# Performance work log

Measured on AMD Instinct MI355X. Metric: run time of the kernel, lower is better.

Reference implementation:

```python
import jax, jax.numpy as jnp
import numpy as np

H = 16   # n_heads == n_I
D = 64   # d_q = d_k = d_v = d_r
DX = H * D
B, S = 4, 2048

def setup_inputs() -> dict:
    key = jax.random.key(0)
    ks = jax.random.split(key, 9)
    sc = 0.02
    return {
        "value": jax.random.normal(ks[0], (B, S, DX), jnp.float32),
        "key":   jax.random.normal(ks[1], (B, S, DX), jnp.float32),
        "query": jax.random.normal(ks[2], (B, S, DX), jnp.float32),
        "Wq_w": jax.random.normal(ks[3], (DX, DX), jnp.float32) * sc,
        "Wq_b": jnp.zeros((DX,), jnp.float32),
        "Wk_w": jax.random.normal(ks[4], (DX, DX), jnp.float32) * sc,
        "Wk_b": jnp.zeros((DX,), jnp.float32),
        "Wv_w": jax.random.normal(ks[5], (DX, DX), jnp.float32) * sc,
        "Wv_b": jnp.zeros((DX,), jnp.float32),
        "Wr_w": jax.random.normal(ks[6], (DX, DX), jnp.float32) * sc,
        "Wr_b": jnp.zeros((DX,), jnp.float32),
        "Wout_w": jax.random.normal(ks[7], (DX, DX), jnp.float32) * sc,
        "Wout_b": jnp.zeros((DX,), jnp.float32),
    }

def _heads(x, b, s):
    # [b, s, H*D] -> [b, H, s, D]
    return x.reshape(b, s, H, D).transpose(0, 2, 1, 3)

def reference(value, key, query, Wq_w, Wq_b, Wk_w, Wk_b, Wv_w, Wv_b,
              Wr_w, Wr_b, Wout_w, Wout_b):
    b, s, _ = query.shape
    # torch nn.Linear: y = x @ W.T + b
    Q = _heads(query @ Wq_w.T + Wq_b, b, s)   # [b,H,s,D]
    K = _heads(key   @ Wk_w.T + Wk_b, b, s)
    V = _heads(value @ Wv_w.T + Wv_b, b, s)
    R = _heads(query @ Wr_w.T + Wr_b, b, s)
    dot_scale = jnp.sqrt(jnp.float32(D))
    scores = jnp.einsum("bhid,bhjd->bhij", Q, K) / dot_scale  # [b,H,s,s]
    attn = jax.nn.softmax(scores, axis=-1)                    # dropout p=0
    out = jnp.einsum("bhij,bhjd->bhid", attn, V)              # [b,H,s,D]
    out = out * R                                             # R-gating
    out = out.transpose(0, 2, 1, 3).reshape(b, s, H * D)
    return out @ Wout_w.T + Wout_b
```

## Files before the change

### kernel.cpp

```cpp
#include <hip/hip_runtime.h>
#include <hip/hip_bf16.h>

typedef __bf16 bf16;
typedef __bf16 bf16x4 __attribute__((ext_vector_type(4)));
typedef __bf16 bf16x8 __attribute__((ext_vector_type(8)));
typedef float  f32x4  __attribute__((ext_vector_type(4)));

#define MFMA_16x16x32(a, b, c) __builtin_amdgcn_mfma_f32_16x16x32_bf16((a), (b), (c), 0, 0, 0)

typedef const void __attribute__((address_space(1))) gvoid;
typedef void __attribute__((address_space(3))) svoid;

__device__ __forceinline__ void async_copy16(const void* gptr, void* ldsptr) {
    __builtin_amdgcn_global_load_lds((gvoid*)gptr, (svoid*)ldsptr, 16, 0, 0);
}

__global__ void cvt_f32_bf16(const float* __restrict__ src, bf16* __restrict__ dst, int n4)
{
    int i = blockIdx.x * blockDim.x + threadIdx.x;
    const int stride = gridDim.x * blockDim.x;
    for (; i < n4; i += stride) {
        float4 v = ((const float4*)src)[i];
        bf16x4 o = { (bf16)v.x, (bf16)v.y, (bf16)v.z, (bf16)v.w };
        ((bf16x4*)dst)[i] = o;
    }
}

template <typename OutT, bool TRANS>
__global__ void gemm_nt_bias(const bf16* __restrict__ X, const bf16* __restrict__ W,
                             const float* __restrict__ bias, OutT* __restrict__ Y,
                             int M, int N, int K)
{
    constexpr int SDIM = 2048;
    __shared__ alignas(16) bf16 As[128 * 32];
    __shared__ alignas(16) bf16 Bs[128 * 32];

    const int tid  = threadIdx.x;
    const int lane = tid & 63;
    const int wave = tid >> 6;
    const int wm   = wave >> 1;
    const int wn   = wave & 1;
    const int bm   = blockIdx.x * 128;
    const int bn   = blockIdx.y * 128;
    const int l15  = lane & 15;
    const int quad = lane >> 4;

    const int srow = lane >> 2;
    const int scol = (lane & 3) * 8;

    const bf16* aseg0 = X + (size_t)(bm + wave * 32 + srow) * K + scol;
    const bf16* aseg1 = X + (size_t)(bm + wave * 32 + 16 + srow) * K + scol;
    const bf16* bseg0 = W + (size_t)(bn + wave * 32 + srow) * K + scol;
    const bf16* bseg1 = W + (size_t)(bn + wave * 32 + 16 + srow) * K + scol;
    bf16* as0 = As + (wave * 2 + 0) * 512;
    bf16* as1 = As + (wave * 2 + 1) * 512;
    bf16* bs0 = Bs + (wave * 2 + 0) * 512;
    bf16* bs1 = Bs + (wave * 2 + 1) * 512;

    f32x4 acc[4][4] = {};

    for (int k0 = 0; k0 < K; k0 += 32) {
        __syncthreads();
        async_copy16(aseg0 + k0, as0);
        async_copy16(aseg1 + k0, as1);
        async_copy16(bseg0 + k0, bs0);
        async_copy16(bseg1 + k0, bs1);
        __syncthreads();

        bf16x8 af[4], bfr[4];
        #pragma unroll
        for (int i = 0; i < 4; ++i)
            af[i] = *(const bf16x8*)(As + (wm * 64 + i * 16 + l15) * 32 + quad * 8);
        #pragma unroll
        for (int j = 0; j < 4; ++j)
            bfr[j] = *(const bf16x8*)(Bs + (wn * 64 + j * 16 + l15) * 32 + quad * 8);
        #pragma unroll
        for (int i = 0; i < 4; ++i)
            #pragma unroll
            for (int j = 0; j < 4; ++j)
                acc[i][j] = MFMA_16x16x32(af[i], bfr[j], acc[i][j]);
    }

    #pragma unroll
    for (int i = 0; i < 4; ++i) {
        const int rowg = bm + wm * 64 + i * 16 + quad * 4;
        #pragma unroll
        for (int j = 0; j < 4; ++j) {
            const int colg = bn + wn * 64 + j * 16 + l15;
            const float bv = bias[colg];
            if (TRANS) {
                bf16x4 o;
                #pragma unroll
                for (int r = 0; r < 4; ++r) o[r] = (bf16)(acc[i][j][r] + bv);
                *(bf16x4*)((bf16*)Y + (size_t)(rowg >> 11) * N * SDIM
                                    + (size_t)colg * SDIM + (rowg & (SDIM - 1))) = o;
            } else {
                #pragma unroll
                for (int r = 0; r < 4; ++r)
                    Y[(size_t)(rowg + r) * N + colg] = (OutT)(acc[i][j][r] + bv);
            }
        }
    }
}

__launch_bounds__(256, 2)
__global__ void attn_fused(const bf16* __restrict__ Qp, const bf16* __restrict__ Kp,
                           const bf16* __restrict__ Vtp, const bf16* __restrict__ Rp,
                           bf16* __restrict__ Op)
{
    constexpr int S = 2048, DXc = 1024, Dh = 64;
    constexpr int PST = 88;
    __shared__ alignas(16) bf16 KsLo[64 * 32], KsHi[64 * 32];
    __shared__ alignas(16) bf16 VtLo[64 * 32], VtHi[64 * 32];
    __shared__ alignas(16) bf16 Pw[4][16 * PST];

    const int tid  = threadIdx.x;
    const int lane = tid & 63;
    const int wave = tid >> 6;
    const int qt = blockIdx.x, h = blockIdx.y, b = blockIdx.z;
    const int l15  = lane & 15;
    const int quad = lane >> 4;

    const size_t headbase = ((size_t)b * S) * DXc + h * Dh;
    const size_t vtbase   = ((size_t)(b * 16 + h) * Dh) * S;

    bf16x8 qf[4][2];
    #pragma unroll
    for (int mi = 0; mi < 4; ++mi) {
        const int qrow = qt * 256 + wave * 64 + mi * 16 + l15;
        const bf16* qptr = Qp + headbase + (size_t)qrow * DXc + quad * 8;
        qf[mi][0] = *(const bf16x8*)(qptr);
        qf[mi][1] = *(const bf16x8*)(qptr + 32);
        #pragma unroll
        for (int j = 0; j < 8; ++j) {
            qf[mi][0][j] = (bf16)((float)qf[mi][0][j] * 0.125f);
            qf[mi][1][j] = (bf16)((float)qf[mi][1][j] * 0.125f);
        }
    }

    f32x4 oacc[4][4] = {};
    float lsum[4][4] = {};

    const int srow = lane >> 2;
    const int scol = (lane & 3) * 8;
    const bf16* kseg = Kp  + headbase + (size_t)(16 * wave + srow) * DXc + scol;
    const bf16* vseg = Vtp + vtbase   + (size_t)(16 * wave + srow) * S   + scol;
    bf16* ksl = KsLo + wave * 512;
    bf16* ksh = KsHi + wave * 512;
    bf16* vtl = VtLo + wave * 512;
    bf16* vth = VtHi + wave * 512;
    bf16* pw  = &Pw[wave][0];

    for (int kv0 = 0; kv0 < S; kv0 += 64) {
        __syncthreads();
        async_copy16(kseg + (size_t)kv0 * DXc,      ksl);
        async_copy16(kseg + (size_t)kv0 * DXc + 32, ksh);
        async_copy16(vseg + kv0,                    vtl);
        async_copy16(vseg + kv0 + 32,               vth);
        __syncthreads();

        bf16x8 kf[4][2], vf[4][2];
        #pragma unroll
        for (int nb = 0; nb < 4; ++nb) {
            kf[nb][0] = *(const bf16x8*)(KsLo + (nb * 16 + l15) * 32 + quad * 8);
            kf[nb][1] = *(const bf16x8*)(KsHi + (nb * 16 + l15) * 32 + quad * 8);
            vf[nb][0] = *(const bf16x8*)(VtLo + (nb * 16 + l15) * 32 + quad * 8);
            vf[nb][1] = *(const bf16x8*)(VtHi + (nb * 16 + l15) * 32 + quad * 8);
        }

        #pragma unroll
        for (int mi = 0; mi < 4; ++mi) {
            f32x4 sacc[4];
            #pragma unroll
            for (int nb = 0; nb < 4; ++nb) {
                f32x4 z = {0.f, 0.f, 0.f, 0.f};
                z = MFMA_16x16x32(qf[mi][1], kf[nb][1], z);
                sacc[nb] = MFMA_16x16x32(qf[mi][0], kf[nb][0], z);
            }
            #pragma unroll
            for (int nb = 0; nb < 4; ++nb) {
                #pragma unroll
                for (int r = 0; r < 4; ++r) {
                    float p = __expf(sacc[nb][r]);
                    bf16 pb = (bf16)p;
                    lsum[mi][r] += (float)pb;
                    pw[(quad * 4 + r) * PST + nb * 16 + l15] = pb;
                }
            }
            bf16x8 pf0 = *(const bf16x8*)(pw + l15 * PST + quad * 8);
            bf16x8 pf1 = *(const bf16x8*)(pw + l15 * PST + 32 + quad * 8);
            #pragma unroll
            for (int db = 0; db < 4; ++db) {
                oacc[mi][db] = MFMA_16x16x32(pf0, vf[db][0], oacc[mi][db]);
                oacc[mi][db] = MFMA_16x16x32(pf1, vf[db][1], oacc[mi][db]);
            }
        }
    }

    #pragma unroll
    for (int m = 1; m < 16; m <<= 1)
        #pragma unroll
        for (int mi = 0; mi < 4; ++mi)
            #pragma unroll
            for (int r = 0; r < 4; ++r)
                lsum[mi][r] += __shfl_xor(lsum[mi][r], m, 64);

    #pragma unroll
    for (int mi = 0; mi < 4; ++mi) {
        #pragma unroll
        for (int r = 0; r < 4; ++r) {
            const float inv = 1.0f / lsum[mi][r];
            const int srowg = qt * 256 + wave * 64 + mi * 16 + quad * 4 + r;
            const size_t base = headbase + (size_t)srowg * DXc;
            #pragma unroll
            for (int db = 0; db < 4; ++db) {
                const int d = db * 16 + l15;
                const float o = oacc[mi][db][r] * inv;
                const float rg = (float)Rp[base + d];
                Op[base + d] = (bf16)(o * rg);
            }
        }
    }
}

extern "C" void kernel_launch(void* const* d_in, const int* in_sizes, int n_in,
                              void* d_out, int out_size, void* d_ws, size_t ws_size,
                              hipStream_t stream)
{
    (void)in_sizes; (void)n_in; (void)out_size; (void)ws_size;
    constexpr int B = 4, S = 2048, DX = 1024, M = B * S;
    constexpr size_t MD = (size_t)M * DX;
    constexpr size_t WD = (size_t)DX * DX;

    const float* value  = (const float*)d_in[0];
    const float* keyi   = (const float*)d_in[1];
    const float* query  = (const float*)d_in[2];
    const float* Wq_w   = (const float*)d_in[3];
    const float* Wq_b   = (const float*)d_in[4];
    const float* Wk_w   = (const float*)d_in[5];
    const float* Wk_b   = (const float*)d_in[6];
    const float* Wv_w   = (const float*)d_in[7];
    const float* Wv_b   = (const float*)d_in[8];
    const float* Wr_w   = (const float*)d_in[9];
    const float* Wr_b   = (const float*)d_in[10];
    const float* Wout_w = (const float*)d_in[11];
    const float* Wout_b = (const float*)d_in[12];

    bf16* p = (bf16*)d_ws;
    bf16* xv = p;            p += MD;
    bf16* xk = p;            p += MD;
    bf16* xq = p;            p += MD;
    bf16* wq = p;            p += WD;
    bf16* wk = p;            p += WD;
    bf16* wv = p;            p += WD;
    bf16* wr = p;            p += WD;
    bf16* wo = p;            p += WD;
    bf16* qws = p;           p += MD;
    bf16* kws = p;           p += MD;
    bf16* vtws = p;          p += MD;
    bf16* rws = p;           p += MD;
    bf16* ows = xv;

    dim3 cblk(256);
    cvt_f32_bf16<<<dim3(1024), cblk, 0, stream>>>(value,  xv, (int)(MD / 4));
    cvt_f32_bf16<<<dim3(1024), cblk, 0, stream>>>(keyi,   xk, (int)(MD / 4));
    cvt_f32_bf16<<<dim3(1024), cblk, 0, stream>>>(query,  xq, (int)(MD / 4));
    cvt_f32_bf16<<<dim3(256),  cblk, 0, stream>>>(Wq_w,   wq, (int)(WD / 4));
    cvt_f32_bf16<<<dim3(256),  cblk, 0, stream>>>(Wk_w,   wk, (int)(WD / 4));
    cvt_f32_bf16<<<dim3(256),  cblk, 0, stream>>>(Wv_w,   wv, (int)(WD / 4));
    cvt_f32_bf16<<<dim3(256),  cblk, 0, stream>>>(Wr_w,   wr, (int)(WD / 4));
    cvt_f32_bf16<<<dim3(256),  cblk, 0, stream>>>(Wout_w, wo, (int)(WD / 4));

    dim3 ggrid(M / 128, DX / 128);
    dim3 gblk(256);

    gemm_nt_bias<bf16, false><<<ggrid, gblk, 0, stream>>>(xq, wq, Wq_b, qws, M, DX, DX);
    gemm_nt_bias<bf16, false><<<ggrid, gblk, 0, stream>>>(xk, wk, Wk_b, kws, M, DX, DX);
    gemm_nt_bias<bf16, true ><<<ggrid, gblk, 0, stream>>>(xv, wv, Wv_b, vtws, M, DX, DX);
    gemm_nt_bias<bf16, false><<<ggrid, gblk, 0, stream>>>(xq, wr, Wr_b, rws, M, DX, DX);

    attn_fused<<<dim3(S / 256, 16, B), gblk, 0, stream>>>(qws, kws, vtws, rws, ows);

    gemm_nt_bias<float, false><<<ggrid, gblk, 0, stream>>>(ows, wo, Wout_b, (float*)d_out, M, DX, DX);
}
```

Measured before the change: 435.4 us.

## Merge Q/R projection GEMM, batch conversions, and retile attention with MFMA row sums

Batches the eight f32-to-bf16 conversion launches into two kernels. Concatenates the Wq and Wr weights so the Q and R projections share one wider GEMM over the query input. In attention, halves the query rows per block (128 instead of 256) so the grid has more blocks and occupancy can rise, folds log2(e) into the Q scale and uses exp2, and computes the softmax denominators with an MFMA against a ones vector instead of scalar adds plus shuffles. The main risks are that the row sum now uses bf16-rounded P through the MFMA path and that each K/V tile is reused by fewer queries.

```diff
diff --git a/kernel.cpp b/kernel.cpp
--- a/kernel.cpp
+++ b/kernel.cpp
@@ -15,14 +15,41 @@
     __builtin_amdgcn_global_load_lds((gvoid*)gptr, (svoid*)ldsptr, 16, 0, 0);
 }
 
-__global__ void cvt_f32_bf16(const float* __restrict__ src, bf16* __restrict__ dst, int n4)
-{
+__global__ void cvt3_acts(const float* __restrict__ s0, const float* __restrict__ s1,
+                          const float* __restrict__ s2,
+                          bf16* __restrict__ d0, bf16* __restrict__ d1, bf16* __restrict__ d2)
+{
+    constexpr int N4SEG = 8192 * 1024 / 4;
     int i = blockIdx.x * blockDim.x + threadIdx.x;
     const int stride = gridDim.x * blockDim.x;
-    for (; i < n4; i += stride) {
-        float4 v = ((const float4*)src)[i];
+    for (; i < 3 * N4SEG; i += stride) {
+        const int seg = i / N4SEG;
+        const int j = i - seg * N4SEG;
+        const float* s = seg == 0 ? s0 : (seg == 1 ? s1 : s2);
+        bf16* d = seg == 0 ? d0 : (seg == 1 ? d1 : d2);
+        float4 v = ((const float4*)s)[j];
         bf16x4 o = { (bf16)v.x, (bf16)v.y, (bf16)v.z, (bf16)v.w };
-        ((bf16x4*)dst)[i] = o;
+        ((bf16x4*)d)[j] = o;
+    }
+}
+
+__global__ void cvt5_wts(const float* __restrict__ s0, const float* __restrict__ s1,
+                         const float* __restrict__ s2, const float* __restrict__ s3,
+                         const float* __restrict__ s4,
+                         bf16* __restrict__ d0, bf16* __restrict__ d1, bf16* __restrict__ d2,
+                         bf16* __restrict__ d3, bf16* __restrict__ d4)
+{
+    constexpr int N4SEG = 1024 * 1024 / 4;
+    int i = blockIdx.x * blockDim.x + threadIdx.x;
+    const int stride = gridDim.x * blockDim.x;
+    for (; i < 5 * N4SEG; i += stride) {
+        const int seg = i / N4SEG;
+        const int j = i - seg * N4SEG;
+        const float* s = seg == 0 ? s0 : seg == 1 ? s1 : seg == 2 ? s2 : seg == 3 ? s3 : s4;
+        bf16* d = seg == 0 ? d0 : seg == 1 ? d1 : seg == 2 ? d2 : seg == 3 ? d3 : d4;
+        float4 v = ((const float4*)s)[j];
+        bf16x4 o = { (bf16)v.x, (bf16)v.y, (bf16)v.z, (bf16)v.w };
+        ((bf16x4*)d)[j] = o;
     }
 }
 
@@ -103,16 +130,15 @@
     }
 }
 
-__launch_bounds__(256, 2)
-__global__ void attn_fused(const bf16* __restrict__ Qp, const bf16* __restrict__ Kp,
-                           const bf16* __restrict__ Vtp, const bf16* __restrict__ Rp,
-                           bf16* __restrict__ Op)
-{
-    constexpr int S = 2048, DXc = 1024, Dh = 64;
+__launch_bounds__(256, 4)
+__global__ void attn_fused(const bf16* __restrict__ QRp, const bf16* __restrict__ Kp,
+                           const bf16* __restrict__ Vtp, bf16* __restrict__ Op)
+{
+    constexpr int S = 2048, DXc = 1024, QRST = 2048, Dh = 64;
     constexpr int PST = 88;
     __shared__ alignas(16) bf16 KsLo[64 * 32], KsHi[64 * 32];
     __shared__ alignas(16) bf16 VtLo[64 * 32], VtHi[64 * 32];
-    __shared__ alignas(16) bf16 Pw[4][16 * PST];
+    __shared__ alignas(16) bf16 Pw[4][2][16 * PST];
 
     const int tid  = threadIdx.x;
     const int lane = tid & 63;
@@ -121,35 +147,41 @@
     const int l15  = lane & 15;
     const int quad = lane >> 4;
 
-    const size_t headbase = ((size_t)b * S) * DXc + h * Dh;
-    const size_t vtbase   = ((size_t)(b * 16 + h) * Dh) * S;
-
-    bf16x8 qf[4][2];
+    const size_t qrbase = ((size_t)b * S) * QRST + h * Dh;
+    const size_t kbase  = ((size_t)b * S) * DXc + h * Dh;
+    const size_t vtbase = ((size_t)(b * 16 + h) * Dh) * S;
+    const size_t obase  = ((size_t)b * S) * DXc + h * Dh;
+
+    constexpr float QSCALE = 0.125f * 1.44269504088896340736f;
+    bf16x8 qf[2][2];
     #pragma unroll
-    for (int mi = 0; mi < 4; ++mi) {
-        const int qrow = qt * 256 + wave * 64 + mi * 16 + l15;
-        const bf16* qptr = Qp + headbase + (size_t)qrow * DXc + quad * 8;
+    for (int mi = 0; mi < 2; ++mi) {
+        const int qrow = qt * 128 + wave * 32 + mi * 16 + l15;
+        const bf16* qptr = QRp + qrbase + (size_t)qrow * QRST + quad * 8;
         qf[mi][0] = *(const bf16x8*)(qptr);
         qf[mi][1] = *(const bf16x8*)(qptr + 32);
         #pragma unroll
         for (int j = 0; j < 8; ++j) {
-            qf[mi][0][j] = (bf16)((float)qf[mi][0][j] * 0.125f);
-            qf[mi][1][j] = (bf16)((float)qf[mi][1][j] * 0.125f);
-        }
-    }
-
-    f32x4 oacc[4][4] = {};
-    float lsum[4][4] = {};
+            qf[mi][0][j] = (bf16)((float)qf[mi][0][j] * QSCALE);
+            qf[mi][1][j] = (bf16)((float)qf[mi][1][j] * QSCALE);
+        }
+    }
+
+    bf16x8 onesf;
+    #pragma unroll
+    for (int j = 0; j < 8; ++j) onesf[j] = (bf16)1.0f;
+
+    f32x4 oacc[2][4] = {};
+    f32x4 lacc[2] = {};
 
     const int srow = lane >> 2;
     const int scol = (lane & 3) * 8;
-    const bf16* kseg = Kp  + headbase + (size_t)(16 * wave + srow) * DXc + scol;
-    const bf16* vseg = Vtp + vtbase   + (size_t)(16 * wave + srow) * S   + scol;
+    const bf16* kseg = Kp  + kbase  + (size_t)(16 * wave + srow) * DXc + scol;
+    const bf16* vseg = Vtp + vtbase + (size_t)(16 * wave + srow) * S   + scol;
     bf16* ksl = KsLo + wave * 512;
     bf16* ksh = KsHi + wave * 512;
     bf16* vtl = VtLo + wave * 512;
     bf16* vth = VtHi + wave * 512;
-    bf16* pw  = &Pw[wave][0];
 
     for (int kv0 = 0; kv0 < S; kv0 += 64) {
         __syncthreads();
@@ -159,65 +191,71 @@
         async_copy16(vseg + kv0 + 32,               vth);
         __syncthreads();
 
-        bf16x8 kf[4][2], vf[4][2];
-        #pragma unroll
-        for (int nb = 0; nb < 4; ++nb) {
-            kf[nb][0] = *(const bf16x8*)(KsLo + (nb * 16 + l15) * 32 + quad * 8);
-            kf[nb][1] = *(const bf16x8*)(KsHi + (nb * 16 + l15) * 32 + quad * 8);
-            vf[nb][0] = *(const bf16x8*)(VtLo + (nb * 16 + l15) * 32 + quad * 8);
-            vf[nb][1] = *(const bf16x8*)(VtHi + (nb * 16 + l15) * 32 + quad * 8);
-        }
-
-        #pragma unroll
-        for (int mi = 0; mi < 4; ++mi) {
-            f32x4 sacc[4];
+        {
+            bf16x8 kf[4][2];
             #pragma unroll
             for (int nb = 0; nb < 4; ++nb) {
-                f32x4 z = {0.f, 0.f, 0.f, 0.f};
-                z = MFMA_16x16x32(qf[mi][1], kf[nb][1], z);
-                sacc[nb] = MFMA_16x16x32(qf[mi][0], kf[nb][0], z);
-            }
+                kf[nb][0] = *(const bf16x8*)(KsLo + (nb * 16 + l15) * 32 + quad * 8);
+                kf[nb][1] = *(const bf16x8*)(KsHi + (nb * 16 + l15) * 32 + quad * 8);
+            }
+            #pragma unroll
+            for (int mi = 0; mi < 2; ++mi) {
+                f32x4 sacc[4];
+                #pragma unroll
+                for (int nb = 0; nb < 4; ++nb) {
+                    f32x4 z = {0.f, 0.f, 0.f, 0.f};
+                    z = MFMA_16x16x32(qf[mi][1], kf[nb][1], z);
+                    sacc[nb] = MFMA_16x16x32(qf[mi][0], kf[nb][0], z);
+                }
+                bf16* pw = &Pw[wave][mi][0];
+                #pragma unroll
+                for (int nb = 0; nb < 4; ++nb) {
+                    #pragma unroll
+                    for (int r = 0; r < 4; ++r) {
+                        float p = __builtin_exp2f(sacc[nb][r]);
+                        pw[(quad * 4 + r) * PST + nb * 16 + l15] = (bf16)p;
+                    }
+                }
+            }
+        }
+
+        {
+            bf16x8 vf[4][2];
             #pragma unroll
             for (int nb = 0; nb < 4; ++nb) {
-                #pragma unroll
-                for (int r = 0; r < 4; ++r) {
-                    float p = __expf(sacc[nb][r]);
-                    bf16 pb = (bf16)p;
-                    lsum[mi][r] += (float)pb;
-                    pw[(quad * 4 + r) * PST + nb * 16 + l15] = pb;
+                vf[nb][0] = *(const bf16x8*)(VtLo + (nb * 16 + l15) * 32 + quad * 8);
+                vf[nb][1] = *(const bf16x8*)(VtHi + (nb * 16 + l15) * 32 + quad * 8);
+            }
+            #pragma unroll
+            for (int mi = 0; mi < 2; ++mi) {
+                const bf16* pw = &Pw[wave][mi][0];
+                bf16x8 pf0 = *(const bf16x8*)(pw + l15 * PST + quad * 8);
+                bf16x8 pf1 = *(const bf16x8*)(pw + l15 * PST + 32 + quad * 8);
+                lacc[mi] = MFMA_16x16x32(pf0, onesf, lacc[mi]);
+                lacc[mi] = MFMA_16x16x32(pf1, onesf, lacc[mi]);
+                #pragma unroll
+                for (int db = 0; db < 4; ++db) {
+                    oacc[mi][db] = MFMA_16x16x32(pf0, vf[db][0], oacc[mi][db]);
+                    oacc[mi][db] = MFMA_16x16x32(pf1, vf[db][1], oacc[mi][db]);
                 }
             }
-            bf16x8 pf0 = *(const bf16x8*)(pw + l15 * PST + quad * 8);
-            bf16x8 pf1 = *(const bf16x8*)(pw + l15 * PST + 32 + quad * 8);
-            #pragma unroll
-            for (int db = 0; db < 4; ++db) {
-                oacc[mi][db] = MFMA_16x16x32(pf0, vf[db][0], oacc[mi][db]);
-                oacc[mi][db] = MFMA_16x16x32(pf1, vf[db][1], oacc[mi][db]);
-            }
         }
     }
 
     #pragma unroll
-    for (int m = 1; m < 16; m <<= 1)
-        #pragma unroll
-        for (int mi = 0; mi < 4; ++mi)
-            #pragma unroll
-            for (int r = 0; r < 4; ++r)
-                lsum[mi][r] += __shfl_xor(lsum[mi][r], m, 64);
-
-    #pragma unroll
-    for (int mi = 0; mi < 4; ++mi) {
+    for (int mi = 0; mi < 2; ++mi) {
         #pragma unroll
         for (int r = 0; r < 4; ++r) {
-            const float inv = 1.0f / lsum[mi][r];
-            const int srowg = qt * 256 + wave * 64 + mi * 16 + quad * 4 + r;
-            const size_t base = headbase + (size_t)srowg * DXc;
+            const float inv = 1.0f / lacc[mi][r];
+            const int row = qt * 128 + wave * 32 + mi * 16 + quad * 4 + r;
+            const bf16* rrow = QRp + qrbase + (size_t)row * QRST + 1024;
+            bf16* orow = Op + obase + (size_t)row * DXc;
             #pragma unroll
             for (int db = 0; db < 4; ++db) {
                 const int d = db * 16 + l15;
                 const float o = oacc[mi][db][r] * inv;
-                const float rg = (float)Rp[base + d];
-                Op[base + d] = (bf16)(o * rg);
+                const float rg = (float)rrow[d];
+                orow[d] = (bf16)(o * rg);
             }
         }
     }
@@ -247,39 +285,36 @@
     const float* Wout_b = (const float*)d_in[12];
 
     bf16* p = (bf16*)d_ws;
-    bf16* xv = p;            p += MD;
-    bf16* xk = p;            p += MD;
-    bf16* xq = p;            p += MD;
-    bf16* wq = p;            p += WD;
-    bf16* wk = p;            p += WD;
-    bf16* wv = p;            p += WD;
-    bf16* wr = p;            p += WD;
-    bf16* wo = p;            p += WD;
-    bf16* qws = p;           p += MD;
-    bf16* kws = p;           p += MD;
-    bf16* vtws = p;          p += MD;
-    bf16* rws = p;           p += MD;
+    bf16* xv  = p;  p += MD;
+    bf16* xk  = p;  p += MD;
+    bf16* xq  = p;  p += MD;
+    bf16* wqr = p;  p += 2 * WD;
+    bf16* wk  = p;  p += WD;
+    bf16* wv  = p;  p += WD;
+    bf16* wo  = p;  p += WD;
+    bf16* qr  = p;  p += 2 * MD;
+    bf16* kws = p;  p += MD;
+    bf16* vtws= p;  p += MD;
+    float* qrb = (float*)p;
     bf16* ows = xv;
 
-    dim3 cblk(256);
-    cvt_f32_bf16<<<dim3(1024), cblk, 0, stream>>>(value,  xv, (int)(MD / 4));
-    cvt_f32_bf16<<<dim3(1024), cblk, 0, stream>>>(keyi,   xk, (int)(MD / 4));
-    cvt_f32_bf16<<<dim3(1024), cblk, 0, stream>>>(query,  xq, (int)(MD / 4));
-    cvt_f32_bf16<<<dim3(256),  cblk, 0, stream>>>(Wq_w,   wq, (int)(WD / 4));
-    cvt_f32_bf16<<<dim3(256),  cblk, 0, stream>>>(Wk_w,   wk, (int)(WD / 4));
-    cvt_f32_bf16<<<dim3(256),  cblk, 0, stream>>>(Wv_w,   wv, (int)(WD / 4));
-    cvt_f32_bf16<<<dim3(256),  cblk, 0, stream>>>(Wr_w,   wr, (int)(WD / 4));
-    cvt_f32_bf16<<<dim3(256),  cblk, 0, stream>>>(Wout_w, wo, (int)(WD / 4));
-
-    dim3 ggrid(M / 128, DX / 128);
+    hipMemcpyAsync(qrb,        Wq_b, DX * sizeof(float), hipMemcpyDeviceToDevice, stream);
+    hipMemcpyAsync(qrb + DX,   Wr_b, DX * sizeof(float), hipMemcpyDeviceToDevice, stream);
+
+    cvt3_acts<<<dim3(2048), dim3(256), 0, stream>>>(value, keyi, query, xv, xk, xq);
+    cvt5_wts <<<dim3(1024), dim3(256), 0, stream>>>(Wq_w, Wr_w, Wk_w, Wv_w, Wout_w,
+                                                    wqr, wqr + WD, wk, wv, wo);
+
     dim3 gblk(256);
-
-    gemm_nt_bias<bf16, false><<<ggrid, gblk, 0, stream>>>(xq, wq, Wq_b, qws, M, DX, DX);
-    gemm_nt_bias<bf16, false><<<ggrid, gblk, 0, stream>>>(xk, wk, Wk_b, kws, M, DX, DX);
-    gemm_nt_bias<bf16, true ><<<ggrid, gblk, 0, stream>>>(xv, wv, Wv_b, vtws, M, DX, DX);
-    gemm_nt_bias<bf16, false><<<ggrid, gblk, 0, stream>>>(xq, wr, Wr_b, rws, M, DX, DX);
-
-    attn_fused<<<dim3(S / 256, 16, B), gblk, 0, stream>>>(qws, kws, vtws, rws, ows);
-
-    gemm_nt_bias<float, false><<<ggrid, gblk, 0, stream>>>(ows, wo, Wout_b, (float*)d_out, M, DX, DX);
-}
+    gemm_nt_bias<bf16, false><<<dim3(M / 128, 2048 / 128), gblk, 0, stream>>>(
+        xq, wqr, qrb, qr, M, 2048, DX);
+    gemm_nt_bias<bf16, false><<<dim3(M / 128, DX / 128), gblk, 0, stream>>>(
+        xk, wk, Wk_b, kws, M, DX, DX);
+    gemm_nt_bias<bf16, true ><<<dim3(M / 128, DX / 128), gblk, 0, stream>>>(
+        xv, wv, Wv_b, vtws, M, DX, DX);
+
+    attn_fused<<<dim3(S / 128, 16, B), gblk, 0, stream>>>(qr, kws, vtws, ows);
+
+    gemm_nt_bias<float, false><<<dim3(M / 128, DX / 128), gblk, 0, stream>>>(
+        ows, wo, Wout_b, (float*)d_out, M, DX, DX);
+}
```

Result: faster. 405.1 us (-6.9%).
